# Kernel tuning notes

Hardware: AMD Instinct MI355X
Metric: run time of the kernel (lower is better)

The kernel has to match this reference:

```python
import jax, jax.numpy as jnp
import numpy as np

NUM_HEADS = 8
CHANNELS = 512


def setup_inputs() -> dict:
    key = jax.random.key(0)
    k1, k2, k3, k4, k5 = jax.random.split(key, 5)
    C = CHANNELS
    x = jax.random.normal(k1, (8, C, 64, 64), dtype=jnp.float32)
    # 1x1 conv weights stored as (out_ch, in_ch) matrices
    qkv_w = jax.random.normal(k2, (3 * C, C), dtype=jnp.float32) * (C ** -0.5)
    qkv_b = jax.random.normal(k3, (3 * C,), dtype=jnp.float32) * 0.02
    proj_w = jax.random.normal(k4, (C, C), dtype=jnp.float32) * (C ** -0.5)
    proj_b = jax.random.normal(k5, (C,), dtype=jnp.float32) * 0.02
    return {"x": x, "qkv_w": qkv_w, "qkv_b": qkv_b, "proj_w": proj_w, "proj_b": proj_b}


def reference(x, qkv_w, qkv_b, proj_w, proj_b):
    B, C, H, W = x.shape
    heads = NUM_HEADS
    d = C // heads
    N = H * W
    scale = d ** -0.5
    # 1x1 conv == per-pixel matmul over channels
    qkv = jnp.einsum('bchw,oc->bohw', x, qkv_w) + qkv_b[None, :, None, None]
    qkv = qkv.reshape(B, 3, heads, d, N)
    q, k, v = qkv[:, 0], qkv[:, 1], qkv[:, 2]  # each (B, heads, d, N)
    # NOTE: attention over the channel dim -> (B, heads, d, d), as in the torch code
    attn = jax.nn.softmax(jnp.einsum('bhdn,bhen->bhde', q, k) * scale, axis=-1)
    # dropout is identity in eval mode
    out = jnp.einsum('bhde,bhen->bhdn', attn, v).reshape(B, C, H, W)
    out = jnp.einsum('bchw,oc->bohw', out, proj_w) + proj_b[None, :, None, None]
    return out, attn.mean(axis=1)  # (B,C,H,W), (B,d,d)
```

## Files before the change

### kernel.cpp

```cpp
#include <hip/hip_runtime.h>
#include <cstdio>
#include <cstdint>

#define BATCH 8
#define CH    512
#define OC3   1536
#define QKROWS 1024
#define NPIX  4096
#define HEADS 8
#define HDIM  64
#define KDEPTH 512
#define SCALE 0.125f
#define NSPLIT 8

typedef __bf16 bf16;
typedef __bf16 bf16x4 __attribute__((ext_vector_type(4)));
typedef __bf16 bf16x8 __attribute__((ext_vector_type(8)));
typedef float  f32x4  __attribute__((ext_vector_type(4)));

#define AS1 __attribute__((address_space(1)))
#define AS3 __attribute__((address_space(3)))

__global__ __launch_bounds__(256) void convert_wvt_kernel(
    const float* __restrict__ qkv_w, bf16* __restrict__ wq_b,
    bf16* __restrict__ wvt)
{
    const int bid = blockIdx.x;
    const int t = threadIdx.x;
    if (bid < (OC3 * KDEPTH) / 256) {
        const int i = bid * 256 + t;
        wq_b[i] = (bf16)qkv_w[i];
        return;
    }
    const int tb = bid - (OC3 * KDEPTH) / 256;
    const int c0 = (tb & 7) * 64;
    const int d0 = (tb >> 3) * 64;
    __shared__ float tl[64][68];
    const float* wv = qkv_w + (size_t)2 * CH * KDEPTH;
    #pragma unroll
    for (int i = 0; i < 4; ++i) {
        const int lin = t + 256 * i;
        const int row = lin >> 4;
        const int c4  = (lin & 15) * 4;
        const float4 v = *(const float4*)(wv + (size_t)(d0 + row) * CH + c0 + c4);
        tl[row][c4 + 0] = v.x; tl[row][c4 + 1] = v.y;
        tl[row][c4 + 2] = v.z; tl[row][c4 + 3] = v.w;
    }
    __syncthreads();
    #pragma unroll
    for (int i = 0; i < 2; ++i) {
        const int lin  = t + 256 * i;
        const int crow = lin >> 3;
        const int d8   = (lin & 7) * 8;
        bf16x8 v;
        #pragma unroll
        for (int j = 0; j < 8; ++j) v[j] = (bf16)tl[d8 + j][crow];
        *(bf16x8*)(wvt + (size_t)(c0 + crow) * CH + d0 + d8) = v;
    }
}

__global__ __launch_bounds__(256) void transpose_convert_kernel(
    const float* __restrict__ src, bf16* __restrict__ dst)
{
    const int b  = blockIdx.z;
    const int n0 = blockIdx.x * 64;
    const int c0 = blockIdx.y * 64;
    __shared__ float tile[64][65];
    const int t = threadIdx.x;
    const float* xp = src + (size_t)b * CH * NPIX;

    #pragma unroll
    for (int i = 0; i < 4; ++i) {
        const int lin = t + 256 * i;
        const int r   = lin >> 4;
        const int c4  = (lin & 15) * 4;
        const float4 v = *(const float4*)(xp + (size_t)(c0 + r) * 4096 + n0 + c4);
        tile[r][c4 + 0] = v.x; tile[r][c4 + 1] = v.y;
        tile[r][c4 + 2] = v.z; tile[r][c4 + 3] = v.w;
    }
    __syncthreads();

    bf16* op = dst + (size_t)b * NPIX * CH;
    #pragma unroll
    for (int i = 0; i < 2; ++i) {
        const int lin = t + 256 * i;
        const int n   = lin >> 3;
        const int c8  = (lin & 7) * 8;
        bf16x8 v;
        #pragma unroll
        for (int jj = 0; jj < 8; ++jj) v[jj] = (bf16)tile[c8 + jj][n];
        *(bf16x8*)(op + (size_t)(n0 + n) * CH + c0 + c8) = v;
    }
}

__global__ __launch_bounds__(256) void gemm_qk_kernel(
    const bf16* __restrict__ A, const bf16* __restrict__ Bt,
    const float* __restrict__ bias, bf16* __restrict__ qkb)
{
    const int nwg  = gridDim.x * gridDim.y;
    const int orig = blockIdx.x + gridDim.x * blockIdx.y;
    const int wg   = (orig & 7) * (nwg >> 3) + (orig >> 3);
    const int by   = wg % gridDim.y;
    const int bx   = wg / gridDim.y;

    const int b  = blockIdx.z;
    const int m0 = by * 128;
    const int n0 = bx * 128;
    const bf16* Ap = A;
    const bf16* Bp = Bt + (size_t)b * NPIX * KDEPTH;

    __shared__ bf16 smem[3 * 8192];

    const int t    = threadIdx.x;
    const int lane = t & 63;
    const int wave = t >> 6;
    const int wr   = wave >> 1, wc = wave & 1;

    f32x4 acc[4][4];
    const f32x4 zf = {0.f, 0.f, 0.f, 0.f};
    #pragma unroll
    for (int i = 0; i < 4; ++i)
        #pragma unroll
        for (int j = 0; j < 4; ++j) acc[i][j] = zf;

    auto STAGE = [&](int tile) {
        bf16* buf = smem + (tile % 3) * 8192;
        const int k0 = tile * 32;
        #pragma unroll
        for (int i = 0; i < 2; ++i) {
            const int c   = t + 256 * i;
            const int row = c >> 2;
            const int kb  = ((c & 3) ^ ((row >> 1) & 3)) * 8;
            __builtin_amdgcn_global_load_lds(
                (const AS1 void*)(Ap + (size_t)(m0 + row) * KDEPTH + k0 + kb),
                (AS3 void*)(buf + c * 8), 16, 0, 0);
            __builtin_amdgcn_global_load_lds(
                (const AS1 void*)(Bp + (size_t)(n0 + row) * KDEPTH + k0 + kb),
                (AS3 void*)(buf + 4096 + c * 8), 16, 0, 0);
        }
    };

    auto COMPUTE = [&](int bufi) {
        const bf16* AsP = smem + bufi * 8192;
        const bf16* BsP = AsP + 4096;
        bf16x8 af[4], bfv[4];
        #pragma unroll
        for (int i = 0; i < 4; ++i) {
            const int ar = wr * 64 + i * 16 + (lane & 15);
            const int ja = (lane >> 4) ^ ((ar >> 1) & 3);
            af[i]  = *(const bf16x8*)(AsP + ar * 32 + ja * 8);
            const int br = wc * 64 + i * 16 + (lane & 15);
            const int jb = (lane >> 4) ^ ((br >> 1) & 3);
            bfv[i] = *(const bf16x8*)(BsP + br * 32 + jb * 8);
        }
        __builtin_amdgcn_s_setprio(1);
        #pragma unroll
        for (int i = 0; i < 4; ++i)
            #pragma unroll
            for (int j = 0; j < 4; ++j)
                acc[i][j] = __builtin_amdgcn_mfma_f32_16x16x32_bf16(
                    af[i], bfv[j], acc[i][j], 0, 0, 0);
        __builtin_amdgcn_s_setprio(0);
    };

    STAGE(0); STAGE(1);
    asm volatile("s_waitcnt vmcnt(4)" ::: "memory");
    asm volatile("s_barrier" ::: "memory");

    int cur = 0;
    for (int kt = 0; kt < 14; ++kt) {
        STAGE(kt + 2);
        COMPUTE(cur);
        __builtin_amdgcn_sched_barrier(0);
        asm volatile("s_waitcnt vmcnt(4)" ::: "memory");
        asm volatile("s_barrier" ::: "memory");
        cur = (cur + 1) % 3;
    }
    COMPUTE(cur);
    __builtin_amdgcn_sched_barrier(0);
    asm volatile("s_waitcnt vmcnt(0)" ::: "memory");
    asm volatile("s_barrier" ::: "memory");
    cur = (cur + 1) % 3;
    COMPUTE(cur);
    __syncthreads();

    {
        bf16* ct = smem;
        #pragma unroll
        for (int i = 0; i < 4; ++i) {
            const int ml = wr * 64 + i * 16 + (lane >> 4) * 4;
            #pragma unroll
            for (int r = 0; r < 4; ++r) {
                const float bv = bias[m0 + ml + r];
                #pragma unroll
                for (int j = 0; j < 4; ++j) {
                    const int n = wc * 64 + j * 16 + (lane & 15);
                    ct[(ml + r) * 128 + n] = (bf16)(acc[i][j][r] + bv);
                }
            }
        }
        __syncthreads();
        bf16* Qp = qkb + (size_t)b * QKROWS * NPIX;
        #pragma unroll
        for (int ii = 0; ii < 8; ++ii) {
            const int c   = t + 256 * ii;
            const int row = c >> 4;
            const int seg = c & 15;
            const int4 v = *(const int4*)(ct + row * 128 + seg * 8);
            *(int4*)(Qp + (size_t)(m0 + row) * NPIX + n0 + seg * 8) = v;
        }
    }
}

__global__ __launch_bounds__(256) void qk_partial_kernel(
    const bf16* __restrict__ qk, float* __restrict__ part)
{
    const int s  = blockIdx.x;
    const int bh = blockIdx.y;
    const int b = bh >> 3, h = bh & 7;
    const bf16* qbase = qk + ((size_t)b * QKROWS + h * HDIM) * NPIX;
    const bf16* kbase = qk + ((size_t)b * QKROWS + CH + h * HDIM) * NPIX;

    __shared__ bf16 smem[16384];

    const int t    = threadIdx.x;
    const int lane = t & 63;
    const int wave = t >> 6;

    f32x4 acc[4];
    const f32x4 zf = {0.f, 0.f, 0.f, 0.f};
    #pragma unroll
    for (int j = 0; j < 4; ++j) acc[j] = zf;

    auto STAGE = [&](int p, int n0) {
        #pragma unroll
        for (int i = 0; i < 2; ++i) {
            const int c   = t + 256 * i;
            const int row = c >> 3;
            const int nb  = ((c & 7) ^ (row & 7)) * 8;
            __builtin_amdgcn_global_load_lds(
                (const AS1 void*)(qbase + (size_t)row * NPIX + n0 + nb),
                (AS3 void*)(smem + p * 8192 + c * 8), 16, 0, 0);
            __builtin_amdgcn_global_load_lds(
                (const AS1 void*)(kbase + (size_t)row * NPIX + n0 + nb),
                (AS3 void*)(smem + p * 8192 + 4096 + c * 8), 16, 0, 0);
        }
    };

    STAGE(0, s * 512);
    __syncthreads();
    int cur = 0;

    for (int nc = 0; nc < 8; ++nc) {
        if (nc < 7) STAGE(cur ^ 1, s * 512 + (nc + 1) * 64);

        const bf16* Qs = smem + cur * 8192;
        const bf16* Ks = Qs + 4096;
        #pragma unroll
        for (int ks = 0; ks < 2; ++ks) {
            const int dr = wave * 16 + (lane & 15);
            const int ja = (ks * 4 + (lane >> 4)) ^ (dr & 7);
            const bf16x8 af = *(const bf16x8*)(Qs + dr * 64 + ja * 8);
            #pragma unroll
            for (int j = 0; j < 4; ++j) {
                const int er = j * 16 + (lane & 15);
                const int jb = (ks * 4 + (lane >> 4)) ^ (er & 7);
                const bf16x8 bf_ = *(const bf16x8*)(Ks + er * 64 + jb * 8);
                acc[j] = __builtin_amdgcn_mfma_f32_16x16x32_bf16(af, bf_, acc[j], 0, 0, 0);
            }
        }
        __syncthreads();
        cur ^= 1;
    }

    float* pb = part + (((size_t)bh * NSPLIT + s) * 64) * 64;
    #pragma unroll
    for (int j = 0; j < 4; ++j)
        #pragma unroll
        for (int r = 0; r < 4; ++r)
            pb[(size_t)(wave * 16 + (lane >> 4) * 4 + r) * 64 + j * 16 + (lane & 15)] = acc[j][r];
}

__global__ __launch_bounds__(256) void qk_reduce_softmax_kernel(
    const float* __restrict__ part, float* __restrict__ attn)
{
    const int bh = blockIdx.x;
    const int t  = threadIdx.x;
    const int r  = t >> 2;
    const int e0 = (t & 3) * 16;

    float v[16];
    #pragma unroll
    for (int i = 0; i < 16; ++i) v[i] = 0.f;

    const float* pb = part + ((size_t)bh * NSPLIT * 64) * 64 + r * 64 + e0;
    for (int s = 0; s < NSPLIT; ++s) {
        const float* ps = pb + (size_t)s * 4096;
        #pragma unroll
        for (int c4 = 0; c4 < 4; ++c4) {
            const float4 p = *(const float4*)(ps + c4 * 4);
            v[c4 * 4 + 0] += p.x; v[c4 * 4 + 1] += p.y;
            v[c4 * 4 + 2] += p.z; v[c4 * 4 + 3] += p.w;
        }
    }

    float m = -1e30f;
    #pragma unroll
    for (int i = 0; i < 16; ++i) m = fmaxf(m, v[i]);
    m = fmaxf(m, __shfl_xor(m, 1));
    m = fmaxf(m, __shfl_xor(m, 2));

    float sum = 0.f;
    #pragma unroll
    for (int i = 0; i < 16; ++i) {
        v[i] = __expf((v[i] - m) * SCALE);
        sum += v[i];
    }
    sum += __shfl_xor(sum, 1);
    sum += __shfl_xor(sum, 2);
    const float inv = 1.f / sum;

    float* arow = attn + ((size_t)bh * 64 + r) * 64 + e0;
    #pragma unroll
    for (int c4 = 0; c4 < 4; ++c4) {
        float4 o;
        o.x = v[c4 * 4 + 0] * inv; o.y = v[c4 * 4 + 1] * inv;
        o.z = v[c4 * 4 + 2] * inv; o.w = v[c4 * 4 + 3] * inv;
        *(float4*)(arow + c4 * 4) = o;
    }
}

__global__ __launch_bounds__(256) void attn_mean_kernel(
    const float* __restrict__ attn, float* __restrict__ om)
{
    const int idx = blockIdx.x * 256 + threadIdx.x;
    const int b = idx >> 12, de = idx & 4095;
    float s = 0.f;
    #pragma unroll
    for (int h = 0; h < 8; ++h)
        s += attn[(((size_t)b * 8 + h) << 12) + de];
    om[idx] = s * 0.125f;
}

__global__ __launch_bounds__(256) void wprime_kernel(
    const float* __restrict__ proj_w, const float* __restrict__ attn,
    bf16* __restrict__ wp)
{
    const int o0 = blockIdx.x * 64;
    const int h  = blockIdx.y;
    const int b  = blockIdx.z;

    __shared__ float ws[64][65];
    __shared__ float as_[64][65];

    const int t = threadIdx.x;
    #pragma unroll
    for (int i = 0; i < 4; ++i) {
        const int lin = t + 256 * i;
        const int r   = lin >> 4;
        const int c4  = (lin & 15) * 4;
        const float4 wv = *(const float4*)(proj_w + (size_t)(o0 + r) * CH + h * HDIM + c4);
        ws[r][c4 + 0] = wv.x; ws[r][c4 + 1] = wv.y;
        ws[r][c4 + 2] = wv.z; ws[r][c4 + 3] = wv.w;
        const float4 av = *(const float4*)(attn + (((size_t)(b * 8 + h) * 64) + r) * 64 + c4);
        as_[r][c4 + 0] = av.x; as_[r][c4 + 1] = av.y;
        as_[r][c4 + 2] = av.z; as_[r][c4 + 3] = av.w;
    }
    __syncthreads();

    const int tx = t & 15, ty = t >> 4;
    const int to = ty * 4, te = tx * 4;
    float acc[4][4] = {};
    for (int d = 0; d < 64; ++d) {
        float a[4], bb[4];
        #pragma unroll
        for (int i = 0; i < 4; ++i) a[i]  = ws[to + i][d];
        #pragma unroll
        for (int j = 0; j < 4; ++j) bb[j] = as_[d][te + j];
        #pragma unroll
        for (int i = 0; i < 4; ++i)
            #pragma unroll
            for (int j = 0; j < 4; ++j)
                acc[i][j] = fmaf(a[i], bb[j], acc[i][j]);
    }

    bf16* wb = wp + (size_t)b * CH * CH;
    #pragma unroll
    for (int i = 0; i < 4; ++i)
        #pragma unroll
        for (int j = 0; j < 4; ++j)
            wb[(size_t)(o0 + to + i) * CH + h * HDIM + te + j] = (bf16)acc[i][j];
}

__global__ __launch_bounds__(256) void bias2_kernel(
    const bf16* __restrict__ wp, const float* __restrict__ bv,
    const float* __restrict__ pb, float* __restrict__ bias2)
{
    const int idx = blockIdx.x * 256 + threadIdx.x;
    const int b = idx >> 9, o = idx & 511;
    const bf16* wr = wp + ((size_t)b * CH + o) * CH;
    float s = 0.f;
    for (int d = 0; d < 512; ++d) s += (float)wr[d] * bv[d];
    bias2[idx] = s + pb[o];
}

__global__ __launch_bounds__(256) void gemm128_kernel(
    const bf16* __restrict__ A, const bf16* __restrict__ Bt,
    const float* __restrict__ bias, size_t bias_bstride,
    float* __restrict__ Cf, bf16* __restrict__ Cb,
    int ncols, int c_rows, size_t a_bstride, size_t bt_bstride)
{
    const int nwg  = gridDim.x * gridDim.y;
    const int orig = blockIdx.x + gridDim.x * blockIdx.y;
    const int wg   = (orig & 7) * (nwg >> 3) + (orig >> 3);
    const int by   = wg % gridDim.y;
    const int bx   = wg / gridDim.y;

    const int b  = blockIdx.z;
    const int m0 = by * 128;
    const int n0 = bx * 128;
    const bf16* Ap = A  + (size_t)b * a_bstride;
    const bf16* Bp = Bt + (size_t)b * bt_bstride;

    __shared__ bf16 smem[3 * 8192];

    const int t    = threadIdx.x;
    const int lane = t & 63;
    const int wave = t >> 6;
    const int wr   = wave >> 1, wc = wave & 1;

    f32x4 acc[4][4];
    const f32x4 zf = {0.f, 0.f, 0.f, 0.f};
    #pragma unroll
    for (int i = 0; i < 4; ++i)
        #pragma unroll
        for (int j = 0; j < 4; ++j) acc[i][j] = zf;

    auto STAGE = [&](int tile) {
        bf16* buf = smem + (tile % 3) * 8192;
        const int k0 = tile * 32;
        #pragma unroll
        for (int i = 0; i < 2; ++i) {
            const int c   = t + 256 * i;
            const int row = c >> 2;
            const int kb  = ((c & 3) ^ ((row >> 1) & 3)) * 8;
            __builtin_amdgcn_global_load_lds(
                (const AS1 void*)(Ap + (size_t)(m0 + row) * KDEPTH + k0 + kb),
                (AS3 void*)(buf + c * 8), 16, 0, 0);
            __builtin_amdgcn_global_load_lds(
                (const AS1 void*)(Bp + (size_t)(n0 + row) * KDEPTH + k0 + kb),
                (AS3 void*)(buf + 4096 + c * 8), 16, 0, 0);
        }
    };

    auto COMPUTE = [&](int bufi) {
        const bf16* AsP = smem + bufi * 8192;
        const bf16* BsP = AsP + 4096;
        bf16x8 af[4], bfv[4];
        #pragma unroll
        for (int i = 0; i < 4; ++i) {
            const int ar = wr * 64 + i * 16 + (lane & 15);
            const int ja = (lane >> 4) ^ ((ar >> 1) & 3);
            af[i]  = *(const bf16x8*)(AsP + ar * 32 + ja * 8);
            const int br = wc * 64 + i * 16 + (lane & 15);
            const int jb = (lane >> 4) ^ ((br >> 1) & 3);
            bfv[i] = *(const bf16x8*)(BsP + br * 32 + jb * 8);
        }
        __builtin_amdgcn_s_setprio(1);
        #pragma unroll
        for (int i = 0; i < 4; ++i)
            #pragma unroll
            for (int j = 0; j < 4; ++j)
                acc[i][j] = __builtin_amdgcn_mfma_f32_16x16x32_bf16(
                    af[i], bfv[j], acc[i][j], 0, 0, 0);
        __builtin_amdgcn_s_setprio(0);
    };

    STAGE(0); STAGE(1);
    asm volatile("s_waitcnt vmcnt(4)" ::: "memory");
    asm volatile("s_barrier" ::: "memory");

    int cur = 0;
    for (int kt = 0; kt < 14; ++kt) {
        STAGE(kt + 2);
        COMPUTE(cur);
        __builtin_amdgcn_sched_barrier(0);
        asm volatile("s_waitcnt vmcnt(4)" ::: "memory");
        asm volatile("s_barrier" ::: "memory");
        cur = (cur + 1) % 3;
    }
    COMPUTE(cur);
    __builtin_amdgcn_sched_barrier(0);
    asm volatile("s_waitcnt vmcnt(0)" ::: "memory");
    asm volatile("s_barrier" ::: "memory");
    cur = (cur + 1) % 3;
    COMPUTE(cur);
    __syncthreads();

    if (Cb) {
        #pragma unroll
        for (int i = 0; i < 4; ++i) {
            const int mb = m0 + wr * 64 + i * 16 + (lane >> 4) * 4;
            #pragma unroll
            for (int r = 0; r < 4; ++r) {
                const int m  = mb + r;
                const float bv = bias ? bias[b * bias_bstride + m] : 0.f;
                #pragma unroll
                for (int j = 0; j < 4; ++j) {
                    const int n = n0 + wc * 64 + j * 16 + (lane & 15);
                    Cb[(size_t)b * c_rows * ncols + (size_t)m * ncols + n] =
                        (bf16)(acc[i][j][r] + bv);
                }
            }
        }
    } else {
        float* ct = (float*)smem;
        float* Cp = Cf + (size_t)b * c_rows * ncols;
        #pragma unroll
        for (int p = 0; p < 2; ++p) {
            if (wc == p) {
                #pragma unroll
                for (int i = 0; i < 4; ++i) {
                    const int ml = wr * 64 + i * 16 + (lane >> 4) * 4;
                    #pragma unroll
                    for (int r = 0; r < 4; ++r) {
                        const float bv = bias ? bias[b * bias_bstride + m0 + ml + r] : 0.f;
                        #pragma unroll
                        for (int j = 0; j < 4; ++j) {
                            const int n = j * 16 + (lane & 15);
                            ct[(ml + r) * 64 + n] = acc[i][j][r] + bv;
                        }
                    }
                }
            }
            __syncthreads();
            #pragma unroll
            for (int ii = 0; ii < 8; ++ii) {
                const int c   = t + 256 * ii;
                const int row = c >> 4;
                const int seg = c & 15;
                const float4 v = *(const float4*)(ct + row * 64 + seg * 4);
                *(float4*)(Cp + (size_t)(m0 + row) * ncols + n0 + p * 64 + seg * 4) = v;
            }
            __syncthreads();
        }
    }
}

extern "C" void kernel_launch(void* const* d_in, const int* in_sizes, int n_in,
                              void* d_out, int out_size, void* d_ws, size_t ws_size,
                              hipStream_t stream)
{
    (void)in_sizes; (void)n_in; (void)out_size;
    const float* x      = (const float*)d_in[0];
    const float* qkv_w  = (const float*)d_in[1];
    const float* qkv_b  = (const float*)d_in[2];
    const float* proj_w = (const float*)d_in[3];
    const float* proj_b = (const float*)d_in[4];

    float* out       = (float*)d_out;
    float* attn_mean = out + (size_t)BATCH * CH * NPIX;

    const size_t qk_bytes   = (size_t)BATCH * QKROWS * NPIX * 2;
    const size_t xt_bytes   = (size_t)BATCH * NPIX * CH * 2;
    const size_t wq_bytes   = (size_t)OC3 * KDEPTH * 2;
    const size_t attn_bytes = (size_t)BATCH * HEADS * HDIM * HDIM * 4;
    const size_t part_bytes = (size_t)BATCH * HEADS * NSPLIT * HDIM * HDIM * 4;
    const size_t wp_bytes   = (size_t)BATCH * CH * CH * 2;
    const size_t wpp_bytes  = (size_t)BATCH * CH * CH * 2;
    const size_t wvt_bytes  = (size_t)CH * CH * 2;
    const size_t b2_bytes   = (size_t)BATCH * CH * 4;
    const size_t need = qk_bytes + xt_bytes + wq_bytes + attn_bytes + part_bytes +
                        wp_bytes + wpp_bytes + wvt_bytes + b2_bytes;
    if (ws_size < need) {
        fprintf(stderr, "[kernel_launch] ws_size=%zu < need=%zu — abort\n", ws_size, need);
        fflush(stderr);
        return;
    }

    char* p = (char*)d_ws;
    bf16*  qk     = (bf16*)p;             p += qk_bytes;
    bf16*  xt     = (bf16*)p;             p += xt_bytes;
    bf16*  wq_b   = (bf16*)p;             p += wq_bytes;
    float* attn   = (float*)p;            p += attn_bytes;
    float* part   = (float*)p;            p += part_bytes;
    bf16*  wprime = (bf16*)p;             p += wp_bytes;
    bf16*  wpp    = (bf16*)p;             p += wpp_bytes;
    bf16*  wvt    = (bf16*)p;             p += wvt_bytes;
    float* bias2  = (float*)p;

    convert_wvt_kernel<<<dim3((OC3 * KDEPTH) / 256 + 64), 256, 0, stream>>>(
        qkv_w, wq_b, wvt);

    transpose_convert_kernel<<<dim3(NPIX / 64, CH / 64, BATCH), 256, 0, stream>>>(x, xt);

    gemm_qk_kernel<<<dim3(NPIX / 128, QKROWS / 128, BATCH), 256, 0, stream>>>(
        wq_b, xt, qkv_b, qk);

    qk_partial_kernel<<<dim3(NSPLIT, BATCH * HEADS), 256, 0, stream>>>(qk, part);
    qk_reduce_softmax_kernel<<<dim3(BATCH * HEADS), 256, 0, stream>>>(part, attn);

    attn_mean_kernel<<<dim3(BATCH * HDIM * HDIM / 256), 256, 0, stream>>>(attn, attn_mean);

    wprime_kernel<<<dim3(CH / 64, HEADS, BATCH), 256, 0, stream>>>(proj_w, attn, wprime);

    gemm128_kernel<<<dim3(CH / 128, CH / 128, BATCH), 256, 0, stream>>>(
        wprime, wvt, nullptr, 0, nullptr, wpp, CH, CH, (size_t)CH * CH, 0);
    bias2_kernel<<<dim3(BATCH * CH / 256), 256, 0, stream>>>(
        wprime, qkv_b + 2 * CH, proj_b, bias2);

    gemm128_kernel<<<dim3(NPIX / 128, CH / 128, BATCH), 256, 0, stream>>>(
        wpp, xt, bias2, CH, out, nullptr, NPIX, CH, (size_t)CH * CH,
        (size_t)NPIX * KDEPTH);
}
```

Baseline: 151.3 us.

## Fuse QK projection GEMM with per-tile Q·Kᵀ partial products

The QK projection GEMM now builds each 128-row A tile from one head's 64 Q rows and 64 K rows. It computes Q·Kᵀ for that 128-pixel tile directly from shared memory and writes a 64x64 float partial per tile. This removes the bf16 round trip of the full Q/K tensor (8x1024x4096) through global memory and drops one kernel launch. The cost is more partials (NSPLIT=32) to reduce, so the softmax reduction is reparallelised across 8 row-groups per head.

```diff
diff --git a/kernel.cpp b/kernel.cpp
--- a/kernel.cpp
+++ b/kernel.cpp
@@ -5,13 +5,12 @@
 #define BATCH 8
 #define CH    512
 #define OC3   1536
-#define QKROWS 1024
 #define NPIX  4096
 #define HEADS 8
 #define HDIM  64
 #define KDEPTH 512
 #define SCALE 0.125f
-#define NSPLIT 8
+#define NSPLIT 32
 
 typedef __bf16 bf16;
 typedef __bf16 bf16x4 __attribute__((ext_vector_type(4)));
@@ -93,20 +92,18 @@
     }
 }
 
-__global__ __launch_bounds__(256) void gemm_qk_kernel(
+__global__ __launch_bounds__(256) void gemm_qks_kernel(
     const bf16* __restrict__ A, const bf16* __restrict__ Bt,
-    const float* __restrict__ bias, bf16* __restrict__ qkb)
+    const float* __restrict__ qkv_b, float* __restrict__ part)
 {
     const int nwg  = gridDim.x * gridDim.y;
     const int orig = blockIdx.x + gridDim.x * blockIdx.y;
     const int wg   = (orig & 7) * (nwg >> 3) + (orig >> 3);
-    const int by   = wg % gridDim.y;
+    const int head = wg % gridDim.y;
     const int bx   = wg / gridDim.y;
 
     const int b  = blockIdx.z;
-    const int m0 = by * 128;
     const int n0 = bx * 128;
-    const bf16* Ap = A;
     const bf16* Bp = Bt + (size_t)b * NPIX * KDEPTH;
 
     __shared__ bf16 smem[3 * 8192];
@@ -129,13 +126,15 @@
         #pragma unroll
         for (int i = 0; i < 2; ++i) {
             const int c   = t + 256 * i;
-            const int row = c >> 2;
-            const int kb  = ((c & 3) ^ ((row >> 1) & 3)) * 8;
+            const int lr  = c >> 2;
+            const int kb  = ((c & 3) ^ ((lr >> 1) & 3)) * 8;
+            const int src = (lr < 64) ? (head * HDIM + lr)
+                                      : (CH + head * HDIM + (lr - 64));
             __builtin_amdgcn_global_load_lds(
-                (const AS1 void*)(Ap + (size_t)(m0 + row) * KDEPTH + k0 + kb),
+                (const AS1 void*)(A + (size_t)src * KDEPTH + k0 + kb),
                 (AS3 void*)(buf + c * 8), 16, 0, 0);
             __builtin_amdgcn_global_load_lds(
-                (const AS1 void*)(Bp + (size_t)(n0 + row) * KDEPTH + k0 + kb),
+                (const AS1 void*)(Bp + (size_t)(n0 + lr) * KDEPTH + k0 + kb),
                 (AS3 void*)(buf + 4096 + c * 8), 16, 0, 0);
         }
     };
@@ -184,150 +183,85 @@
     COMPUTE(cur);
     __syncthreads();
 
-    {
-        bf16* ct = smem;
-        #pragma unroll
-        for (int i = 0; i < 4; ++i) {
-            const int ml = wr * 64 + i * 16 + (lane >> 4) * 4;
-            #pragma unroll
-            for (int r = 0; r < 4; ++r) {
-                const float bv = bias[m0 + ml + r];
-                #pragma unroll
-                for (int j = 0; j < 4; ++j) {
-                    const int n = wc * 64 + j * 16 + (lane & 15);
-                    ct[(ml + r) * 128 + n] = (bf16)(acc[i][j][r] + bv);
-                }
-            }
-        }
-        __syncthreads();
-        bf16* Qp = qkb + (size_t)b * QKROWS * NPIX;
-        #pragma unroll
-        for (int ii = 0; ii < 8; ++ii) {
-            const int c   = t + 256 * ii;
-            const int row = c >> 4;
-            const int seg = c & 15;
-            const int4 v = *(const int4*)(ct + row * 128 + seg * 8);
-            *(int4*)(Qp + (size_t)(m0 + row) * NPIX + n0 + seg * 8) = v;
-        }
-    }
-}
-
-__global__ __launch_bounds__(256) void qk_partial_kernel(
-    const bf16* __restrict__ qk, float* __restrict__ part)
-{
-    const int s  = blockIdx.x;
-    const int bh = blockIdx.y;
-    const int b = bh >> 3, h = bh & 7;
-    const bf16* qbase = qk + ((size_t)b * QKROWS + h * HDIM) * NPIX;
-    const bf16* kbase = qk + ((size_t)b * QKROWS + CH + h * HDIM) * NPIX;
-
-    __shared__ bf16 smem[16384];
-
-    const int t    = threadIdx.x;
-    const int lane = t & 63;
-    const int wave = t >> 6;
-
-    f32x4 acc[4];
-    const f32x4 zf = {0.f, 0.f, 0.f, 0.f};
-    #pragma unroll
-    for (int j = 0; j < 4; ++j) acc[j] = zf;
-
-    auto STAGE = [&](int p, int n0) {
-        #pragma unroll
-        for (int i = 0; i < 2; ++i) {
-            const int c   = t + 256 * i;
-            const int row = c >> 3;
-            const int nb  = ((c & 7) ^ (row & 7)) * 8;
-            __builtin_amdgcn_global_load_lds(
-                (const AS1 void*)(qbase + (size_t)row * NPIX + n0 + nb),
-                (AS3 void*)(smem + p * 8192 + c * 8), 16, 0, 0);
-            __builtin_amdgcn_global_load_lds(
-                (const AS1 void*)(kbase + (size_t)row * NPIX + n0 + nb),
-                (AS3 void*)(smem + p * 8192 + 4096 + c * 8), 16, 0, 0);
-        }
-    };
-
-    STAGE(0, s * 512);
-    __syncthreads();
-    int cur = 0;
-
-    for (int nc = 0; nc < 8; ++nc) {
-        if (nc < 7) STAGE(cur ^ 1, s * 512 + (nc + 1) * 64);
-
-        const bf16* Qs = smem + cur * 8192;
-        const bf16* Ks = Qs + 4096;
-        #pragma unroll
-        for (int ks = 0; ks < 2; ++ks) {
-            const int dr = wave * 16 + (lane & 15);
-            const int ja = (ks * 4 + (lane >> 4)) ^ (dr & 7);
-            const bf16x8 af = *(const bf16x8*)(Qs + dr * 64 + ja * 8);
+    bf16* ct = smem;
+    #pragma unroll
+    for (int i = 0; i < 4; ++i) {
+        const int mlb = wr * 64 + i * 16 + (lane >> 4) * 4;
+        #pragma unroll
+        for (int r = 0; r < 4; ++r) {
+            const int row = mlb + r;
+            const int bsrc = (row < 64) ? (head * HDIM + row)
+                                        : (CH + head * HDIM + (row - 64));
+            const float bv = qkv_b[bsrc];
             #pragma unroll
             for (int j = 0; j < 4; ++j) {
-                const int er = j * 16 + (lane & 15);
-                const int jb = (ks * 4 + (lane >> 4)) ^ (er & 7);
-                const bf16x8 bf_ = *(const bf16x8*)(Ks + er * 64 + jb * 8);
-                acc[j] = __builtin_amdgcn_mfma_f32_16x16x32_bf16(af, bf_, acc[j], 0, 0, 0);
+                const int n = wc * 64 + j * 16 + (lane & 15);
+                ct[row * 128 + (((n >> 3) ^ (row & 15)) * 8) + (n & 7)] =
+                    (bf16)(acc[i][j][r] + bv);
             }
         }
-        __syncthreads();
-        cur ^= 1;
-    }
-
-    float* pb = part + (((size_t)bh * NSPLIT + s) * 64) * 64;
-    #pragma unroll
-    for (int j = 0; j < 4; ++j)
+    }
+    __syncthreads();
+
+    f32x4 sacc[4];
+    #pragma unroll
+    for (int df = 0; df < 4; ++df) sacc[df] = zf;
+    #pragma unroll
+    for (int ks = 0; ks < 4; ++ks) {
+        const int slot8 = ((ks * 4 + (lane >> 4)) ^ (lane & 15)) * 8;
+        const bf16x8 kf = *(const bf16x8*)(ct + (64 + wave * 16 + (lane & 15)) * 128 + slot8);
+        #pragma unroll
+        for (int df = 0; df < 4; ++df) {
+            const bf16x8 qf = *(const bf16x8*)(ct + (df * 16 + (lane & 15)) * 128 + slot8);
+            sacc[df] = __builtin_amdgcn_mfma_f32_16x16x32_bf16(qf, kf, sacc[df], 0, 0, 0);
+        }
+    }
+
+    float* pp = part + (((size_t)(b * 8 + head) * NSPLIT + bx) * 64) * 64;
+    #pragma unroll
+    for (int df = 0; df < 4; ++df)
         #pragma unroll
         for (int r = 0; r < 4; ++r)
-            pb[(size_t)(wave * 16 + (lane >> 4) * 4 + r) * 64 + j * 16 + (lane & 15)] = acc[j][r];
+            pp[(size_t)(df * 16 + (lane >> 4) * 4 + r) * 64 + wave * 16 + (lane & 15)]
+                = sacc[df][r];
 }
 
 __global__ __launch_bounds__(256) void qk_reduce_softmax_kernel(
     const float* __restrict__ part, float* __restrict__ attn)
 {
-    const int bh = blockIdx.x;
+    const int rg = blockIdx.x, bh = blockIdx.y;
     const int t  = threadIdx.x;
-    const int r  = t >> 2;
-    const int e0 = (t & 3) * 16;
-
-    float v[16];
-    #pragma unroll
-    for (int i = 0; i < 16; ++i) v[i] = 0.f;
-
-    const float* pb = part + ((size_t)bh * NSPLIT * 64) * 64 + r * 64 + e0;
+    const int row = rg * 8 + (t >> 5);
+    const int le  = t & 31;
+
+    const float* pb = part + (size_t)bh * NSPLIT * 4096 + row * 64;
+    float v0 = 0.f, v1 = 0.f;
+    #pragma unroll 8
     for (int s = 0; s < NSPLIT; ++s) {
-        const float* ps = pb + (size_t)s * 4096;
-        #pragma unroll
-        for (int c4 = 0; c4 < 4; ++c4) {
-            const float4 p = *(const float4*)(ps + c4 * 4);
-            v[c4 * 4 + 0] += p.x; v[c4 * 4 + 1] += p.y;
-            v[c4 * 4 + 2] += p.z; v[c4 * 4 + 3] += p.w;
-        }
-    }
-
-    float m = -1e30f;
-    #pragma unroll
-    for (int i = 0; i < 16; ++i) m = fmaxf(m, v[i]);
+        v0 += pb[(size_t)s * 4096 + le];
+        v1 += pb[(size_t)s * 4096 + 32 + le];
+    }
+
+    float m = fmaxf(v0, v1);
     m = fmaxf(m, __shfl_xor(m, 1));
     m = fmaxf(m, __shfl_xor(m, 2));
-
-    float sum = 0.f;
-    #pragma unroll
-    for (int i = 0; i < 16; ++i) {
-        v[i] = __expf((v[i] - m) * SCALE);
-        sum += v[i];
-    }
+    m = fmaxf(m, __shfl_xor(m, 4));
+    m = fmaxf(m, __shfl_xor(m, 8));
+    m = fmaxf(m, __shfl_xor(m, 16));
+
+    v0 = __expf((v0 - m) * SCALE);
+    v1 = __expf((v1 - m) * SCALE);
+    float sum = v0 + v1;
     sum += __shfl_xor(sum, 1);
     sum += __shfl_xor(sum, 2);
+    sum += __shfl_xor(sum, 4);
+    sum += __shfl_xor(sum, 8);
+    sum += __shfl_xor(sum, 16);
     const float inv = 1.f / sum;
 
-    float* arow = attn + ((size_t)bh * 64 + r) * 64 + e0;
-    #pragma unroll
-    for (int c4 = 0; c4 < 4; ++c4) {
-        float4 o;
-        o.x = v[c4 * 4 + 0] * inv; o.y = v[c4 * 4 + 1] * inv;
-        o.z = v[c4 * 4 + 2] * inv; o.w = v[c4 * 4 + 3] * inv;
-        *(float4*)(arow + c4 * 4) = o;
-    }
+    float* arow = attn + ((size_t)bh * 64 + row) * 64;
+    arow[le]      = v0 * inv;
+    arow[32 + le] = v1 * inv;
 }
 
 __global__ __launch_bounds__(256) void attn_mean_kernel(
@@ -561,16 +495,15 @@
     float* out       = (float*)d_out;
     float* attn_mean = out + (size_t)BATCH * CH * NPIX;
 
-    const size_t qk_bytes   = (size_t)BATCH * QKROWS * NPIX * 2;
     const size_t xt_bytes   = (size_t)BATCH * NPIX * CH * 2;
+    const size_t part_bytes = (size_t)BATCH * HEADS * NSPLIT * HDIM * HDIM * 4;
     const size_t wq_bytes   = (size_t)OC3 * KDEPTH * 2;
     const size_t attn_bytes = (size_t)BATCH * HEADS * HDIM * HDIM * 4;
-    const size_t part_bytes = (size_t)BATCH * HEADS * NSPLIT * HDIM * HDIM * 4;
     const size_t wp_bytes   = (size_t)BATCH * CH * CH * 2;
     const size_t wpp_bytes  = (size_t)BATCH * CH * CH * 2;
     const size_t wvt_bytes  = (size_t)CH * CH * 2;
     const size_t b2_bytes   = (size_t)BATCH * CH * 4;
-    const size_t need = qk_bytes + xt_bytes + wq_bytes + attn_bytes + part_bytes +
+    const size_t need = xt_bytes + part_bytes + wq_bytes + attn_bytes +
                         wp_bytes + wpp_bytes + wvt_bytes + b2_bytes;
     if (ws_size < need) {
         fprintf(stderr, "[kernel_launch] ws_size=%zu < need=%zu — abort\n", ws_size, need);
@@ -579,11 +512,10 @@
     }
 
     char* p = (char*)d_ws;
-    bf16*  qk     = (bf16*)p;             p += qk_bytes;
     bf16*  xt     = (bf16*)p;             p += xt_bytes;
+    float* part   = (float*)p;            p += part_bytes;
     bf16*  wq_b   = (bf16*)p;             p += wq_bytes;
     float* attn   = (float*)p;            p += attn_bytes;
-    float* part   = (float*)p;            p += part_bytes;
     bf16*  wprime = (bf16*)p;             p += wp_bytes;
     bf16*  wpp    = (bf16*)p;             p += wpp_bytes;
     bf16*  wvt    = (bf16*)p;             p += wvt_bytes;
@@ -594,11 +526,10 @@
 
     transpose_convert_kernel<<<dim3(NPIX / 64, CH / 64, BATCH), 256, 0, stream>>>(x, xt);
 
-    gemm_qk_kernel<<<dim3(NPIX / 128, QKROWS / 128, BATCH), 256, 0, stream>>>(
-        wq_b, xt, qkv_b, qk);
-
-    qk_partial_kernel<<<dim3(NSPLIT, BATCH * HEADS), 256, 0, stream>>>(qk, part);
-    qk_reduce_softmax_kernel<<<dim3(BATCH * HEADS), 256, 0, stream>>>(part, attn);
+    gemm_qks_kernel<<<dim3(NPIX / 128, HEADS, BATCH), 256, 0, stream>>>(
+        wq_b, xt, qkv_b, part);
+
+    qk_reduce_softmax_kernel<<<dim3(8, BATCH * HEADS), 256, 0, stream>>>(part, attn);
 
     attn_mean_kernel<<<dim3(BATCH * HDIM * HDIM / 256), 256, 0, stream>>>(attn, attn_mean);
 
```

New measurement: 140.8 us. 1.07x faster.
